# Kernel tuning notes

Hardware: AMD Instinct MI355X
Metric: run time of the kernel (lower is better)

Reference implementation:

```python
import jax, jax.numpy as jnp
import numpy as np

NX, NY, NZ = 432, 496, 1
C = 64
B = 4
P = 64000


def setup_inputs() -> dict:
    key = jax.random.key(0)
    k1, k2, k3 = jax.random.split(key, 3)
    pillar_features = jax.random.normal(k1, (P, C), dtype=jnp.float32)
    # Build unique (batch, y, x) cells so the scatter has no duplicate targets
    # (torch advanced-index assignment with duplicates is order-dependent).
    n_cells = B * NY * NX
    flat = jax.random.permutation(k2, n_cells)[:P]  # unique global cell ids
    b = flat // (NY * NX)
    rem = flat % (NY * NX)
    y = rem // NX
    x = rem % NX
    z = jnp.zeros_like(b)
    voxel_coords = jnp.stack([b, z, y, x], axis=1).astype(jnp.int32)  # [P, 4]
    return {
        "pillar_features": pillar_features,
        "voxel_coords": voxel_coords,
        "batch_size": B,
    }


def reference(pillar_features, voxel_coords, batch_size):
    # Global scatter: one fused pass instead of the per-batch Python loop.
    coords = voxel_coords.astype(jnp.int32)
    # per-sample spatial index, exactly as in the torch code: z + y*nx + x
    spatial_idx = coords[:, 1] + coords[:, 2] * NX + coords[:, 3]
    global_idx = coords[:, 0] * (NY * NX) + spatial_idx  # [P]
    canvas = jnp.zeros((batch_size * NZ * NY * NX, pillar_features.shape[1]),
                       dtype=pillar_features.dtype)
    canvas = canvas.at[global_idx].set(pillar_features)  # [B*ny*nx, C]
    # -> [B, C, ny, nx], matching view(batch, C*nz, ny, nx)
    spatial = canvas.reshape(batch_size, NY, NX, -1).transpose(0, 3, 1, 2)
    return spatial
```

## Files before the change

### kernel.cpp

```cpp
#include <hip/hip_runtime.h>

#define PNX 432
#define PNY 496
#define PNC 64
#define PLANE (PNY * PNX)

typedef float f32x4 __attribute__((ext_vector_type(4)));


__global__ void pp_scatter_map(const int4* __restrict__ coords,
                               int* __restrict__ map, int P) {
    int p = blockIdx.x * blockDim.x + threadIdx.x;
    if (p >= P) return;
    int4 c = coords[p];
    int gidx = c.x * PLANE + c.y + c.z * PNX + c.w;
    map[gidx] = p;
}

__global__ void pp_gather(const float* __restrict__ feat,
                          const int* __restrict__ map,
                          float* __restrict__ out, int n4) {
    int t = blockIdx.x * blockDim.x + threadIdx.x;
    if (t >= n4) return;
    int cell0 = t * 4;
    int b = cell0 / PLANE;
    int spat = cell0 - b * PLANE;
    int cbase = blockIdx.y * (PNC / 4);

    int4 pm = *reinterpret_cast<const int4*>(map + cell0);
    const f32x4* fp0 = reinterpret_cast<const f32x4*>(feat + (long)pm.x * PNC + cbase);
    const f32x4* fp1 = reinterpret_cast<const f32x4*>(feat + (long)pm.y * PNC + cbase);
    const f32x4* fp2 = reinterpret_cast<const f32x4*>(feat + (long)pm.z * PNC + cbase);
    const f32x4* fp3 = reinterpret_cast<const f32x4*>(feat + (long)pm.w * PNC + cbase);

    float* outp = out + (size_t)b * PNC * PLANE + (size_t)cbase * PLANE + spat;
    const f32x4 z = {0.f, 0.f, 0.f, 0.f};

    #pragma unroll
    for (int g = 0; g < 4; ++g) {
        f32x4 r0 = (pm.x >= 0) ? fp0[g] : z;
        f32x4 r1 = (pm.y >= 0) ? fp1[g] : z;
        f32x4 r2 = (pm.z >= 0) ? fp2[g] : z;
        f32x4 r3 = (pm.w >= 0) ? fp3[g] : z;
        f32x4 o0 = {r0.x, r1.x, r2.x, r3.x};
        f32x4 o1 = {r0.y, r1.y, r2.y, r3.y};
        f32x4 o2 = {r0.z, r1.z, r2.z, r3.z};
        f32x4 o3 = {r0.w, r1.w, r2.w, r3.w};
        float* o = outp + (size_t)(g * 4) * PLANE;
        __builtin_nontemporal_store(o0, reinterpret_cast<f32x4*>(o));
        __builtin_nontemporal_store(o1, reinterpret_cast<f32x4*>(o + PLANE));
        __builtin_nontemporal_store(o2, reinterpret_cast<f32x4*>(o + 2 * PLANE));
        __builtin_nontemporal_store(o3, reinterpret_cast<f32x4*>(o + 3 * PLANE));
    }
}


__global__ void pp_zero_out(f32x4* __restrict__ out4, size_t n4) {
    size_t t = (size_t)blockIdx.x * blockDim.x + threadIdx.x;
    size_t stride = (size_t)gridDim.x * blockDim.x;
    const f32x4 z = {0.f, 0.f, 0.f, 0.f};
    for (size_t i = t; i < n4; i += stride) out4[i] = z;
}

__global__ void pp_scatter_direct(const float* __restrict__ feat,
                                  const int4* __restrict__ coords,
                                  float* __restrict__ out, int P) {
    int t = blockIdx.x * blockDim.x + threadIdx.x;
    int p = t >> 6;
    int c = t & 63;
    if (p >= P) return;
    int4 co = coords[p];
    size_t oidx = ((size_t)(co.x * PNC + c)) * PLANE + co.y + co.z * PNX + co.w;
    out[oidx] = feat[p * PNC + c];
}

extern "C" void kernel_launch(void* const* d_in, const int* in_sizes, int n_in,
                              void* d_out, int out_size, void* d_ws, size_t ws_size,
                              hipStream_t stream) {
    const float* feat = (const float*)d_in[0];
    const int4* coords = (const int4*)d_in[1];
    float* out = (float*)d_out;

    const int P = in_sizes[0] / PNC;
    const int B = out_size / (PNC * PLANE);
    const int ncells = B * PLANE;
    const size_t mapBytes = (size_t)ncells * sizeof(int);

    if (ws_size >= mapBytes) {
        int* map = (int*)d_ws;
        int n4 = ncells / 4;
        (void)hipMemsetAsync(map, 0xFF, mapBytes, stream);
        pp_scatter_map<<<(P + 255) / 256, 256, 0, stream>>>(coords, map, P);
        dim3 grid((n4 + 255) / 256, 4);
        pp_gather<<<grid, 256, 0, stream>>>(feat, map, out, n4);
    } else {
        size_t n4 = (size_t)out_size / 4;
        pp_zero_out<<<2048, 256, 0, stream>>>((f32x4*)out, n4);
        int total = P * PNC;
        pp_scatter_direct<<<(total + 255) / 256, 256, 0, stream>>>(feat, coords, out, P);
    }
}
```

Before: 55.34 us.

## Gather one cell per thread with scalar stores and a zero-row source

Each gather thread now handles a single cell and all 64 channels: it reads the full feature row (or a shared zero row when the cell is empty) and writes 64 scalar stores strided by plane. This replaces the previous scheme of 4 cells × 16 channels per thread with 16-byte nontemporal stores. The hipMemset is also replaced with a custom init kernel that fills the map and zeroes the row. The aim is to remove the per-cell branch and the register transpose, but stores shrink from 16-byte vectors to 4-byte scalars and the nontemporal hints are dropped.

```diff
diff --git a/kernel.cpp b/kernel.cpp
--- a/kernel.cpp
+++ b/kernel.cpp
@@ -7,6 +7,11 @@
 
 typedef float f32x4 __attribute__((ext_vector_type(4)));
 
+__global__ void pp_init(int4* __restrict__ map4, float* __restrict__ zrow, int n4) {
+    int t = blockIdx.x * blockDim.x + threadIdx.x;
+    if (t < n4) map4[t] = make_int4(-1, -1, -1, -1);
+    if (blockIdx.x == 0 && threadIdx.x < PNC) zrow[threadIdx.x] = 0.0f;
+}
 
 __global__ void pp_scatter_map(const int4* __restrict__ coords,
                                int* __restrict__ map, int P) {
@@ -19,38 +24,28 @@
 
 __global__ void pp_gather(const float* __restrict__ feat,
                           const int* __restrict__ map,
-                          float* __restrict__ out, int n4) {
-    int t = blockIdx.x * blockDim.x + threadIdx.x;
-    if (t >= n4) return;
-    int cell0 = t * 4;
-    int b = cell0 / PLANE;
-    int spat = cell0 - b * PLANE;
-    int cbase = blockIdx.y * (PNC / 4);
+                          const float* __restrict__ zrow,
+                          float* __restrict__ out, int ncells) {
+    int cell = blockIdx.x * blockDim.x + threadIdx.x;
+    if (cell >= ncells) return;
+    int b = cell / PLANE;
+    int spat = cell - b * PLANE;
+    int pm = map[cell];
 
-    int4 pm = *reinterpret_cast<const int4*>(map + cell0);
-    const f32x4* fp0 = reinterpret_cast<const f32x4*>(feat + (long)pm.x * PNC + cbase);
-    const f32x4* fp1 = reinterpret_cast<const f32x4*>(feat + (long)pm.y * PNC + cbase);
-    const f32x4* fp2 = reinterpret_cast<const f32x4*>(feat + (long)pm.z * PNC + cbase);
-    const f32x4* fp3 = reinterpret_cast<const f32x4*>(feat + (long)pm.w * PNC + cbase);
+    const float* src = (pm >= 0) ? (feat + (size_t)pm * PNC) : zrow;
+    const f32x4* fp = reinterpret_cast<const f32x4*>(src);
 
-    float* outp = out + (size_t)b * PNC * PLANE + (size_t)cbase * PLANE + spat;
-    const f32x4 z = {0.f, 0.f, 0.f, 0.f};
+    f32x4 r[16];
+    #pragma unroll
+    for (int g = 0; g < 16; ++g) r[g] = fp[g];
 
+    float* o = out + (size_t)b * PNC * PLANE + spat;
     #pragma unroll
-    for (int g = 0; g < 4; ++g) {
-        f32x4 r0 = (pm.x >= 0) ? fp0[g] : z;
-        f32x4 r1 = (pm.y >= 0) ? fp1[g] : z;
-        f32x4 r2 = (pm.z >= 0) ? fp2[g] : z;
-        f32x4 r3 = (pm.w >= 0) ? fp3[g] : z;
-        f32x4 o0 = {r0.x, r1.x, r2.x, r3.x};
-        f32x4 o1 = {r0.y, r1.y, r2.y, r3.y};
-        f32x4 o2 = {r0.z, r1.z, r2.z, r3.z};
-        f32x4 o3 = {r0.w, r1.w, r2.w, r3.w};
-        float* o = outp + (size_t)(g * 4) * PLANE;
-        __builtin_nontemporal_store(o0, reinterpret_cast<f32x4*>(o));
-        __builtin_nontemporal_store(o1, reinterpret_cast<f32x4*>(o + PLANE));
-        __builtin_nontemporal_store(o2, reinterpret_cast<f32x4*>(o + 2 * PLANE));
-        __builtin_nontemporal_store(o3, reinterpret_cast<f32x4*>(o + 3 * PLANE));
+    for (int g = 0; g < 16; ++g) {
+        o[(size_t)(4 * g + 0) * PLANE] = r[g].x;
+        o[(size_t)(4 * g + 1) * PLANE] = r[g].y;
+        o[(size_t)(4 * g + 2) * PLANE] = r[g].z;
+        o[(size_t)(4 * g + 3) * PLANE] = r[g].w;
     }
 }
 
@@ -85,14 +80,15 @@
     const int B = out_size / (PNC * PLANE);
     const int ncells = B * PLANE;
     const size_t mapBytes = (size_t)ncells * sizeof(int);
+    const size_t needBytes = mapBytes + PNC * sizeof(float);
 
-    if (ws_size >= mapBytes) {
+    if (ws_size >= needBytes) {
         int* map = (int*)d_ws;
+        float* zrow = (float*)((char*)d_ws + mapBytes);
         int n4 = ncells / 4;
-        (void)hipMemsetAsync(map, 0xFF, mapBytes, stream);
+        pp_init<<<(n4 + 255) / 256, 256, 0, stream>>>((int4*)map, zrow, n4);
         pp_scatter_map<<<(P + 255) / 256, 256, 0, stream>>>(coords, map, P);
-        dim3 grid((n4 + 255) / 256, 4);
-        pp_gather<<<grid, 256, 0, stream>>>(feat, map, out, n4);
+        pp_gather<<<(ncells + 255) / 256, 256, 0, stream>>>(feat, map, zrow, out, ncells);
     } else {
         size_t n4 = (size_t)out_size / 4;
         pp_zero_out<<<2048, 256, 0, stream>>>((f32x4*)out, n4);
```

New measurement: 46.04 us. 16.8% less time.
